# Performance work log

Hardware: AMD Instinct MI355X
Metric: run time of the kernel (lower is better)

The kernel has to match this reference:

```python
import jax, jax.numpy as jnp
import numpy as np

D_MODEL = 512
SEQ_LEN = 2048
S = 32  # local window size
BATCH = 2


def setup_inputs() -> dict:
    key = jax.random.key(0)
    ks = jax.random.split(key, 12)
    shp = (SEQ_LEN, BATCH, D_MODEL)
    return {
        "query": jax.random.normal(ks[0], shp, jnp.float32),
        "key": jax.random.normal(ks[1], shp, jnp.float32),
        "value": jax.random.normal(ks[2], shp, jnp.float32),
        "Wq": jax.random.normal(ks[3], (D_MODEL, D_MODEL), jnp.float32) * 0.02,
        "bq": jax.random.normal(ks[4], (D_MODEL,), jnp.float32) * 0.01,
        "Wk": jax.random.normal(ks[5], (D_MODEL, D_MODEL), jnp.float32) * 0.02,
        "bk": jax.random.normal(ks[6], (D_MODEL,), jnp.float32) * 0.01,
        "Wv": jax.random.normal(ks[7], (D_MODEL, D_MODEL), jnp.float32) * 0.02,
        "bv": jax.random.normal(ks[8], (D_MODEL,), jnp.float32) * 0.01,
        "pos_bias": jax.random.normal(ks[9], (SEQ_LEN, SEQ_LEN), jnp.float32) * 0.02,
        "Wo": jax.random.normal(ks[10], (D_MODEL, D_MODEL), jnp.float32) * 0.02,
        "bo": jax.random.normal(ks[11], (D_MODEL,), jnp.float32) * 0.01,
    }


def _aft_local(query, key, value, Wq, bq, Wk, bk, Wv, bv, pos_bias, Wo, bo):
    T, B, D = query.shape
    q = query @ Wq.T + bq  # [T,B,D]
    k = key @ Wk.T + bk
    v = value @ Wv.T + bv
    pb = pos_bias[:T, :T]

    # max_logit: elementwise max of per-dim key max and (key + col-max of pos_bias) max,
    # then batch index 0 (faithful to original `[0]` indexing) -> shape [D]
    max_logit = jnp.maximum(k.max(axis=0),
                            (k + pb.max(axis=0)[:, None, None]).max(axis=0))[0]

    # out-of-window running sums: tokens t' <= t - S contribute exp(k) (no pos bias)
    ek = jnp.exp(k - max_logit)                 # [T,B,D]
    cs_num = jnp.cumsum(ek * v, axis=0)
    cs_den = jnp.cumsum(ek, axis=0)
    t_arr = jnp.arange(T)
    prefix_idx = jnp.clip(t_arr - S, 0, T - 1)
    has_prefix = (t_arr >= S)[:, None, None]
    num_out = jnp.where(has_prefix, cs_num[prefix_idx], 0.0)
    den_out = jnp.where(has_prefix, cs_den[prefix_idx], 0.0)

    # in-window part: t' in [max(0, t-S+1), t] with pos_bias[t, t']
    j = jnp.arange(S)
    idx_raw = t_arr[:, None] - S + 1 + j[None, :]   # [T,S]
    valid = (idx_raw >= 0).astype(k.dtype)
    idx = jnp.clip(idx_raw, 0, T - 1)
    k_win = k[idx]                                  # [T,S,B,D]
    v_win = v[idx]                                  # [T,S,B,D]
    pb_win = pb[t_arr[:, None], idx]                # [T,S]
    exp_l = jnp.exp(k_win + pb_win[:, :, None, None] - max_logit) * valid[:, :, None, None]
    num_in = (exp_l * v_win).sum(axis=1)            # [T,B,D]
    den_in = exp_l.sum(axis=1)

    y = jax.nn.sigmoid(q) * (num_out + num_in) / (den_out + den_in)
    return y @ Wo.T + bo


def reference(query, key, value, Wq, bq, Wk, bk, Wv, bv, pos_bias, Wo, bo):
    return _aft_local(query, key, value, Wq, bq, Wk, bk, Wv, bv, pos_bias, Wo, bo)
```

## Files before the change

### kernel.cpp

```cpp
#include <hip/hip_runtime.h>
#include <hip/hip_bf16.h>

#define TT 2048
#define BB 2
#define DD 512
#define BD (BB*DD)
#define SS 32
#define MR (TT*BB)
#define NE (TT*BB*DD)
#define CH 32

typedef __bf16 bf16x8 __attribute__((ext_vector_type(8)));
typedef float f32x4 __attribute__((ext_vector_type(4)));

__device__ __forceinline__ void async_copy16(void* lds, const void* gptr) {
    __builtin_amdgcn_global_load_lds(
        (const __attribute__((address_space(1))) void*)gptr,
        (__attribute__((address_space(3))) void*)lds,
        16, 0, 0);
}

#define MFMA16(a,b,c) __builtin_amdgcn_mfma_f32_16x16x32_bf16((a),(b),(c),0,0,0)

__global__ __launch_bounds__(256) void cast_all(
    const float* __restrict__ s0, const float* __restrict__ s1, const float* __restrict__ s2,
    const float* __restrict__ w0, const float* __restrict__ w1,
    const float* __restrict__ w2, const float* __restrict__ w3,
    __hip_bfloat16* __restrict__ d0, __hip_bfloat16* __restrict__ d1, __hip_bfloat16* __restrict__ d2,
    __hip_bfloat16* __restrict__ e0, __hip_bfloat16* __restrict__ e1,
    __hip_bfloat16* __restrict__ e2, __hip_bfloat16* __restrict__ e3)
{
    int b = blockIdx.x;
    const float* s;
    __hip_bfloat16* d;
    size_t i;
    if (b < 6144) {
        int which = b >> 11;
        s = which == 0 ? s0 : (which == 1 ? s1 : s2);
        d = which == 0 ? d0 : (which == 1 ? d1 : d2);
        i = ((size_t)(b & 2047) * 256 + threadIdx.x) * 4;
    } else {
        int b2 = b - 6144;
        int which = b2 >> 8;
        s = which == 0 ? w0 : (which == 1 ? w1 : (which == 2 ? w2 : w3));
        d = which == 0 ? e0 : (which == 1 ? e1 : (which == 2 ? e2 : e3));
        i = ((size_t)(b2 & 255) * 256 + threadIdx.x) * 4;
    }
    float4 f = *(const float4*)(s + i);
    union { __hip_bfloat16 h[4]; ushort4 u; } cv;
    cv.h[0] = __float2bfloat16(f.x); cv.h[1] = __float2bfloat16(f.y);
    cv.h[2] = __float2bfloat16(f.z); cv.h[3] = __float2bfloat16(f.w);
    *(ushort4*)((unsigned short*)d + i) = cv.u;
}

__global__ __launch_bounds__(256) void gemm_qkv(
    const __hip_bfloat16* __restrict__ qb, const __hip_bfloat16* __restrict__ kb,
    const __hip_bfloat16* __restrict__ vb,
    const __hip_bfloat16* __restrict__ Wqb, const __hip_bfloat16* __restrict__ Wkb,
    const __hip_bfloat16* __restrict__ Wvb,
    const float* __restrict__ bq, const float* __restrict__ bk,
    const float* __restrict__ bv,
    float* __restrict__ qout, float* __restrict__ ekn,
    float* __restrict__ part)
{
    __shared__ char smem[49152];
    const int tid = threadIdx.x;
    const int lane = tid & 63;
    const int wv = tid >> 6;
    const int wave_m = wv >> 1, wave_n = wv & 1;
    const int m0 = blockIdx.y * 64, n0 = blockIdx.x * 64;
    const int kq = lane >> 4, rr = lane & 15;

    if (blockIdx.z == 0) {
        f32x4 acc[2][2] = {};
        const __hip_bfloat16* Arow = qb + (size_t)(m0 + lane) * DD + wv * 8;
        const __hip_bfloat16* Wrow = Wqb + (size_t)(n0 + lane) * DD + wv * 8;
        async_copy16(smem + 0*8192 +        wv*1024, Arow + 0);
        async_copy16(smem + 0*8192 + 4096 + wv*1024, Wrow + 0);
        async_copy16(smem + 1*8192 +        wv*1024, Arow + 32);
        async_copy16(smem + 1*8192 + 4096 + wv*1024, Wrow + 32);
        asm volatile("s_waitcnt vmcnt(2)" ::: "memory");
        __builtin_amdgcn_s_barrier();
        #pragma unroll
        for (int it = 0; it < 16; ++it) {
            if (it + 2 < 16) {
                char* nb = smem + ((it + 2) % 3) * 8192;
                async_copy16(nb +        wv*1024, Arow + (it+2)*32);
                async_copy16(nb + 4096 + wv*1024, Wrow + (it+2)*32);
            }
            const char* cb = smem + (it % 3) * 8192;
            bf16x8 a0 = *(const bf16x8*)(cb + kq*1024 + (wave_m*32 +  0 + rr)*16);
            bf16x8 a1 = *(const bf16x8*)(cb + kq*1024 + (wave_m*32 + 16 + rr)*16);
            bf16x8 w0 = *(const bf16x8*)(cb + 4096 + kq*1024 + (wave_n*32 +  0 + rr)*16);
            bf16x8 w1 = *(const bf16x8*)(cb + 4096 + kq*1024 + (wave_n*32 + 16 + rr)*16);
            acc[0][0] = MFMA16(a0, w0, acc[0][0]);
            acc[0][1] = MFMA16(a0, w1, acc[0][1]);
            acc[1][0] = MFMA16(a1, w0, acc[1][0]);
            acc[1][1] = MFMA16(a1, w1, acc[1][1]);
            if (it < 15) {
                if (it < 14) asm volatile("s_waitcnt vmcnt(2) lgkmcnt(0)" ::: "memory");
                else         asm volatile("s_waitcnt vmcnt(0) lgkmcnt(0)" ::: "memory");
                __builtin_amdgcn_s_barrier();
            }
        }
        #pragma unroll
        for (int ms = 0; ms < 2; ++ms)
            #pragma unroll
            for (int ns = 0; ns < 2; ++ns) {
                int n = n0 + wave_n*32 + ns*16 + rr;
                float bn = bq[n];
                #pragma unroll
                for (int r = 0; r < 4; ++r) {
                    int m = m0 + wave_m*32 + ms*16 + kq*4 + r;
                    qout[(size_t)m * DD + n] = acc[ms][ns][r] + bn;
                }
            }
    } else {
        f32x4 acck[2][2] = {}, accv[2][2] = {};
        const __hip_bfloat16* AKrow = kb + (size_t)(m0 + lane) * DD + wv * 8;
        const __hip_bfloat16* WKrow = Wkb + (size_t)(n0 + lane) * DD + wv * 8;
        const __hip_bfloat16* AVrow = vb + (size_t)(m0 + lane) * DD + wv * 8;
        const __hip_bfloat16* WVrow = Wvb + (size_t)(n0 + lane) * DD + wv * 8;
        #pragma unroll
        for (int pt = 0; pt < 2; ++pt) {
            char* nb = smem + pt * 16384;
            async_copy16(nb +         wv*1024, AKrow + pt*32);
            async_copy16(nb +  4096 + wv*1024, WKrow + pt*32);
            async_copy16(nb +  8192 + wv*1024, AVrow + pt*32);
            async_copy16(nb + 12288 + wv*1024, WVrow + pt*32);
        }
        asm volatile("s_waitcnt vmcnt(4)" ::: "memory");
        __builtin_amdgcn_s_barrier();
        #pragma unroll
        for (int it = 0; it < 16; ++it) {
            if (it + 2 < 16) {
                char* nb = smem + ((it + 2) % 3) * 16384;
                async_copy16(nb +         wv*1024, AKrow + (it+2)*32);
                async_copy16(nb +  4096 + wv*1024, WKrow + (it+2)*32);
                async_copy16(nb +  8192 + wv*1024, AVrow + (it+2)*32);
                async_copy16(nb + 12288 + wv*1024, WVrow + (it+2)*32);
            }
            const char* cb = smem + (it % 3) * 16384;
            bf16x8 ak0 = *(const bf16x8*)(cb +         kq*1024 + (wave_m*32 +  0 + rr)*16);
            bf16x8 ak1 = *(const bf16x8*)(cb +         kq*1024 + (wave_m*32 + 16 + rr)*16);
            bf16x8 bk0 = *(const bf16x8*)(cb +  4096 + kq*1024 + (wave_n*32 +  0 + rr)*16);
            bf16x8 bk1 = *(const bf16x8*)(cb +  4096 + kq*1024 + (wave_n*32 + 16 + rr)*16);
            bf16x8 av0 = *(const bf16x8*)(cb +  8192 + kq*1024 + (wave_m*32 +  0 + rr)*16);
            bf16x8 av1 = *(const bf16x8*)(cb +  8192 + kq*1024 + (wave_m*32 + 16 + rr)*16);
            bf16x8 bv0 = *(const bf16x8*)(cb + 12288 + kq*1024 + (wave_n*32 +  0 + rr)*16);
            bf16x8 bv1 = *(const bf16x8*)(cb + 12288 + kq*1024 + (wave_n*32 + 16 + rr)*16);
            acck[0][0] = MFMA16(ak0, bk0, acck[0][0]);
            acck[0][1] = MFMA16(ak0, bk1, acck[0][1]);
            acck[1][0] = MFMA16(ak1, bk0, acck[1][0]);
            acck[1][1] = MFMA16(ak1, bk1, acck[1][1]);
            accv[0][0] = MFMA16(av0, bv0, accv[0][0]);
            accv[0][1] = MFMA16(av0, bv1, accv[0][1]);
            accv[1][0] = MFMA16(av1, bv0, accv[1][0]);
            accv[1][1] = MFMA16(av1, bv1, accv[1][1]);
            if (it < 15) {
                if (it < 14) asm volatile("s_waitcnt vmcnt(4) lgkmcnt(0)" ::: "memory");
                else         asm volatile("s_waitcnt vmcnt(0) lgkmcnt(0)" ::: "memory");
                __builtin_amdgcn_s_barrier();
            }
        }
        float sd[2][2] = {{0.f,0.f},{0.f,0.f}};
        float sn[2][2] = {{0.f,0.f},{0.f,0.f}};
        #pragma unroll
        for (int ms = 0; ms < 2; ++ms)
            #pragma unroll
            for (int ns = 0; ns < 2; ++ns) {
                int n = n0 + wave_n*32 + ns*16 + rr;
                float bkn = bk[n], bvn = bv[n];
                #pragma unroll
                for (int r = 0; r < 4; ++r) {
                    int m = m0 + wave_m*32 + ms*16 + kq*4 + r;
                    float e  = expf(acck[ms][ns][r] + bkn);
                    float nv = e * (accv[ms][ns][r] + bvn);
                    float2 st; st.x = e; st.y = nv;
                    *(float2*)&ekn[((size_t)m * DD + n) * 2] = st;
                    sd[ns][r & 1] += e;
                    sn[ns][r & 1] += nv;
                }
            }
        #pragma unroll
        for (int ns = 0; ns < 2; ++ns)
            #pragma unroll
            for (int par = 0; par < 2; ++par) {
                sd[ns][par] += __shfl_xor(sd[ns][par], 16, 64);
                sd[ns][par] += __shfl_xor(sd[ns][par], 32, 64);
                sn[ns][par] += __shfl_xor(sn[ns][par], 16, 64);
                sn[ns][par] += __shfl_xor(sn[ns][par], 32, 64);
            }
        __syncthreads();
        float* red = (float*)smem;
        if (lane < 16) {
            #pragma unroll
            for (int ns = 0; ns < 2; ++ns) {
                int c = wave_n*32 + ns*16 + rr;
                red[(0*2 + wave_m)*64 + c] = sd[ns][0];
                red[(1*2 + wave_m)*64 + c] = sd[ns][1];
                red[(2*2 + wave_m)*64 + c] = sn[ns][0];
                red[(3*2 + wave_m)*64 + c] = sn[ns][1];
            }
        }
        __syncthreads();
        {
            int which = tid >> 6;
            int c = tid & 63;
            float s = red[(which*2 + 0)*64 + c] + red[(which*2 + 1)*64 + c];
            int b = which & 1;
            int sel = which >> 1;
            part[((size_t)blockIdx.y * BD + b*512 + n0 + c) * 2 + sel] = s;
        }
    }
}

__global__ __launch_bounds__(256) void fused_window(
    const float* __restrict__ q, const float* __restrict__ ekn,
    const float* __restrict__ part, const float* __restrict__ pb,
    __hip_bfloat16* __restrict__ yb)
{
    __shared__ float wl[CH][SS];
    const int tid = threadIdx.x;
    const int col = blockIdx.x * 256 + tid;
    const int chunk = blockIdx.y;
    const int t0 = chunk * CH;

    #pragma unroll
    for (int i = 0; i < (CH * SS) / 256; ++i) {
        int idx = tid + i * 256;
        int tl = idx >> 5, j = idx & 31;
        int t = t0 + tl;
        int u = t - (SS - 1) + j;
        float w = 0.f;
        if (u >= 0) w = expf(pb[(size_t)t * TT + u]);
        wl[tl][j] = w;
    }
    __syncthreads();

    float ring_d[32], ring_n[32];
    float cs_d = 0.f, cs_n = 0.f;
    const bool hasp = (chunk > 0);
    if (hasp) {
        float pd[4] = {0.f,0.f,0.f,0.f}, pn[4] = {0.f,0.f,0.f,0.f};
        int p = 0;
        for (; p + 4 <= chunk; p += 4) {
            #pragma unroll
            for (int u2 = 0; u2 < 4; ++u2) {
                float2 v = *(const float2*)&part[((size_t)(p + u2) * BD + col) * 2];
                pd[u2] += v.x; pn[u2] += v.y;
            }
        }
        for (; p < chunk; ++p) {
            float2 v = *(const float2*)&part[((size_t)p * BD + col) * 2];
            pd[0] += v.x; pn[0] += v.y;
        }
        float pref_d = (pd[0] + pd[1]) + (pd[2] + pd[3]);
        float pref_n = (pn[0] + pn[1]) + (pn[2] + pn[3]);
        float ssd = 0.f, ssn = 0.f;
        #pragma unroll
        for (int i = 0; i < 32; ++i) {
            float2 v = *(const float2*)&ekn[((size_t)(t0 - 32 + i) * BD + col) * 2];
            ring_d[i] = v.x; ring_n[i] = v.y;
            ssd += v.x; ssn += v.y;
        }
        cs_d = pref_d - ssd;
        cs_n = pref_n - ssn;
    } else {
        #pragma unroll
        for (int i = 0; i < 32; ++i) { ring_d[i] = 0.f; ring_n[i] = 0.f; }
    }

    #pragma unroll
    for (int s = 0; s < CH; ++s) {
        int t = t0 + s;
        size_t off = (size_t)t * BD + col;
        float2 env = *(const float2*)&ekn[off * 2];
        cs_d += ring_d[s];
        cs_n += ring_n[s];
        ring_d[s] = env.x;
        ring_n[s] = env.y;
        float den = 0.f, num = 0.f;
        #pragma unroll
        for (int j4 = 0; j4 < 8; ++j4) {
            float4 w4 = *(const float4*)&wl[s][j4 * 4];
            den += w4.x * ring_d[(s + 1 + j4*4 + 0) & 31];
            num += w4.x * ring_n[(s + 1 + j4*4 + 0) & 31];
            den += w4.y * ring_d[(s + 1 + j4*4 + 1) & 31];
            num += w4.y * ring_n[(s + 1 + j4*4 + 1) & 31];
            den += w4.z * ring_d[(s + 1 + j4*4 + 2) & 31];
            num += w4.z * ring_n[(s + 1 + j4*4 + 2) & 31];
            den += w4.w * ring_d[(s + 1 + j4*4 + 3) & 31];
            num += w4.w * ring_n[(s + 1 + j4*4 + 3) & 31];
        }
        if (hasp) { den += cs_d; num += cs_n; }
        float qv = q[off];
        float sig = 1.f / (1.f + expf(-qv));
        yb[off] = __float2bfloat16(sig * num / den);
    }
}

__global__ __launch_bounds__(256) void gemm_out(
    const __hip_bfloat16* __restrict__ yb, const __hip_bfloat16* __restrict__ Wob,
    const float* __restrict__ bo, float* __restrict__ out)
{
    __shared__ char smem[24576];
    const int tid = threadIdx.x;
    const int lane = tid & 63;
    const int wv = tid >> 6;
    const int wave_m = wv >> 1, wave_n = wv & 1;
    const int m0 = blockIdx.y * 64, n0 = blockIdx.x * 64;
    const int kq = lane >> 4, rr = lane & 15;

    f32x4 acc[2][2] = {};
    const __hip_bfloat16* Arow = yb + (size_t)(m0 + lane) * DD + wv * 8;
    const __hip_bfloat16* Wrow = Wob + (size_t)(n0 + lane) * DD + wv * 8;

    async_copy16(smem + 0*8192 +        wv*1024, Arow + 0);
    async_copy16(smem + 0*8192 + 4096 + wv*1024, Wrow + 0);
    async_copy16(smem + 1*8192 +        wv*1024, Arow + 32);
    async_copy16(smem + 1*8192 + 4096 + wv*1024, Wrow + 32);
    asm volatile("s_waitcnt vmcnt(2)" ::: "memory");
    __builtin_amdgcn_s_barrier();
    #pragma unroll
    for (int it = 0; it < 16; ++it) {
        if (it + 2 < 16) {
            char* nb = smem + ((it + 2) % 3) * 8192;
            async_copy16(nb +        wv*1024, Arow + (it+2)*32);
            async_copy16(nb + 4096 + wv*1024, Wrow + (it+2)*32);
        }
        const char* cb = smem + (it % 3) * 8192;
        bf16x8 a0 = *(const bf16x8*)(cb + kq*1024 + (wave_m*32 +  0 + rr)*16);
        bf16x8 a1 = *(const bf16x8*)(cb + kq*1024 + (wave_m*32 + 16 + rr)*16);
        bf16x8 w0 = *(const bf16x8*)(cb + 4096 + kq*1024 + (wave_n*32 +  0 + rr)*16);
        bf16x8 w1 = *(const bf16x8*)(cb + 4096 + kq*1024 + (wave_n*32 + 16 + rr)*16);
        acc[0][0] = MFMA16(a0, w0, acc[0][0]);
        acc[0][1] = MFMA16(a0, w1, acc[0][1]);
        acc[1][0] = MFMA16(a1, w0, acc[1][0]);
        acc[1][1] = MFMA16(a1, w1, acc[1][1]);
        if (it < 15) {
            if (it < 14) asm volatile("s_waitcnt vmcnt(2) lgkmcnt(0)" ::: "memory");
            else         asm volatile("s_waitcnt vmcnt(0) lgkmcnt(0)" ::: "memory");
            __builtin_amdgcn_s_barrier();
        }
    }
    #pragma unroll
    for (int ms = 0; ms < 2; ++ms)
        #pragma unroll
        for (int ns = 0; ns < 2; ++ns) {
            int n = n0 + wave_n*32 + ns*16 + rr;
            float bn = bo[n];
            #pragma unroll
            for (int r = 0; r < 4; ++r) {
                int m = m0 + wave_m*32 + ms*16 + kq*4 + r;
                out[(size_t)m * DD + n] = acc[ms][ns][r] + bn;
            }
        }
}

extern "C" void kernel_launch(void* const* d_in, const int* in_sizes, int n_in,
                              void* d_out, int out_size, void* d_ws, size_t ws_size,
                              hipStream_t stream) {
    const float* query = (const float*)d_in[0];
    const float* key   = (const float*)d_in[1];
    const float* value = (const float*)d_in[2];
    const float* Wq    = (const float*)d_in[3];
    const float* bq    = (const float*)d_in[4];
    const float* Wk    = (const float*)d_in[5];
    const float* bk    = (const float*)d_in[6];
    const float* Wv    = (const float*)d_in[7];
    const float* bv    = (const float*)d_in[8];
    const float* pb    = (const float*)d_in[9];
    const float* Wo    = (const float*)d_in[10];
    const float* bo    = (const float*)d_in[11];
    float* out = (float*)d_out;

    float* ws = (float*)d_ws;
    float* q    = ws;
    float* ekn  = ws + (size_t)NE;
    float* part = ws + (size_t)3 * NE;
    __hip_bfloat16* bfb = (__hip_bfloat16*)(part + 131072);
    __hip_bfloat16* qb  = bfb;
    __hip_bfloat16* kb  = bfb + (size_t)NE;
    __hip_bfloat16* vb  = bfb + (size_t)2 * NE;
    __hip_bfloat16* yb  = bfb + (size_t)3 * NE;
    __hip_bfloat16* Wqb = bfb + (size_t)4 * NE;
    __hip_bfloat16* Wkb = Wqb + 262144;
    __hip_bfloat16* Wvb = Wkb + 262144;
    __hip_bfloat16* Wob = Wvb + 262144;

    cast_all<<<7168, 256, 0, stream>>>(query, key, value, Wq, Wk, Wv, Wo,
                                       qb, kb, vb, Wqb, Wkb, Wvb, Wob);

    gemm_qkv<<<dim3(DD / 64, MR / 64, 2), 256, 0, stream>>>(
        qb, kb, vb, Wqb, Wkb, Wvb, bq, bk, bv,
        q, ekn, part);

    fused_window<<<dim3(BD / 256, TT / CH), 256, 0, stream>>>(
        q, ekn, part, pb, yb);

    gemm_out<<<dim3(DD / 64, MR / 64), 256, 0, stream>>>(yb, Wob, bo, out);
}
```

Baseline: 172.0 us.

## Precompute chunk prefix sums in a separate scan kernel and preload window registers

Adds a small scan_part kernel that turns the per-chunk partial sums into exclusive prefix sums. fused_window then reads one prefix value instead of summing up to 63 partials per column, which removes the quadratic reduction across chunks. The fused kernel also loads all 64 ekn values and 32 q values into registers up front and uses vector float2 arithmetic. The costs are an extra kernel launch, a tiny 4-block kernel that runs serially, and higher register pressure (launch_bounds 256,1).

```diff
diff --git a/kernel.cpp b/kernel.cpp
--- a/kernel.cpp
+++ b/kernel.cpp
@@ -12,6 +12,7 @@
 
 typedef __bf16 bf16x8 __attribute__((ext_vector_type(8)));
 typedef float f32x4 __attribute__((ext_vector_type(4)));
+typedef float f32x2 __attribute__((ext_vector_type(2)));
 
 __device__ __forceinline__ void async_copy16(void* lds, const void* gptr) {
     __builtin_amdgcn_global_load_lds(
@@ -215,9 +216,28 @@
     }
 }
 
-__global__ __launch_bounds__(256) void fused_window(
+__global__ __launch_bounds__(256, 1) void scan_part(
+    const float* __restrict__ part, float* __restrict__ pref)
+{
+    const int col = blockIdx.x * 256 + threadIdx.x;
+    f32x2 run = {0.f, 0.f};
+    #pragma unroll
+    for (int p0 = 0; p0 < 64; p0 += 8) {
+        f32x2 v[8];
+        #pragma unroll
+        for (int u = 0; u < 8; ++u)
+            v[u] = *(const f32x2*)&part[((size_t)(p0 + u) * BD + col) * 2];
+        #pragma unroll
+        for (int u = 0; u < 8; ++u) {
+            *(f32x2*)&pref[((size_t)(p0 + u) * BD + col) * 2] = run;
+            run += v[u];
+        }
+    }
+}
+
+__global__ __launch_bounds__(256, 1) void fused_window(
     const float* __restrict__ q, const float* __restrict__ ekn,
-    const float* __restrict__ part, const float* __restrict__ pb,
+    const float* __restrict__ pref, const float* __restrict__ pb,
     __hip_bfloat16* __restrict__ yb)
 {
     __shared__ float wl[CH][SS];
@@ -225,6 +245,24 @@
     const int col = blockIdx.x * 256 + tid;
     const int chunk = blockIdx.y;
     const int t0 = chunk * CH;
+
+    f32x2 E[64];
+    if (chunk > 0) {
+        #pragma unroll
+        for (int i = 0; i < 64; ++i)
+            E[i] = *(const f32x2*)&ekn[((size_t)(t0 - 32 + i) * BD + col) * 2];
+    } else {
+        #pragma unroll
+        for (int i = 0; i < 32; ++i) E[i] = (f32x2){0.f, 0.f};
+        #pragma unroll
+        for (int i = 32; i < 64; ++i)
+            E[i] = *(const f32x2*)&ekn[((size_t)(t0 - 32 + i) * BD + col) * 2];
+    }
+    f32x2 P = *(const f32x2*)&pref[((size_t)chunk * BD + col) * 2];
+    float qv[CH];
+    #pragma unroll
+    for (int s = 0; s < CH; ++s)
+        qv[s] = q[(size_t)(t0 + s) * BD + col];
 
     #pragma unroll
     for (int i = 0; i < (CH * SS) / 256; ++i) {
@@ -238,65 +276,24 @@
     }
     __syncthreads();
 
-    float ring_d[32], ring_n[32];
-    float cs_d = 0.f, cs_n = 0.f;
-    const bool hasp = (chunk > 0);
-    if (hasp) {
-        float pd[4] = {0.f,0.f,0.f,0.f}, pn[4] = {0.f,0.f,0.f,0.f};
-        int p = 0;
-        for (; p + 4 <= chunk; p += 4) {
-            #pragma unroll
-            for (int u2 = 0; u2 < 4; ++u2) {
-                float2 v = *(const float2*)&part[((size_t)(p + u2) * BD + col) * 2];
-                pd[u2] += v.x; pn[u2] += v.y;
-            }
-        }
-        for (; p < chunk; ++p) {
-            float2 v = *(const float2*)&part[((size_t)p * BD + col) * 2];
-            pd[0] += v.x; pn[0] += v.y;
-        }
-        float pref_d = (pd[0] + pd[1]) + (pd[2] + pd[3]);
-        float pref_n = (pn[0] + pn[1]) + (pn[2] + pn[3]);
-        float ssd = 0.f, ssn = 0.f;
-        #pragma unroll
-        for (int i = 0; i < 32; ++i) {
-            float2 v = *(const float2*)&ekn[((size_t)(t0 - 32 + i) * BD + col) * 2];
-            ring_d[i] = v.x; ring_n[i] = v.y;
-            ssd += v.x; ssn += v.y;
-        }
-        cs_d = pref_d - ssd;
-        cs_n = pref_n - ssn;
-    } else {
-        #pragma unroll
-        for (int i = 0; i < 32; ++i) { ring_d[i] = 0.f; ring_n[i] = 0.f; }
-    }
+    f32x2 cs = P;
+    #pragma unroll
+    for (int i = 0; i < 32; ++i) cs -= E[i];
 
     #pragma unroll
     for (int s = 0; s < CH; ++s) {
-        int t = t0 + s;
-        size_t off = (size_t)t * BD + col;
-        float2 env = *(const float2*)&ekn[off * 2];
-        cs_d += ring_d[s];
-        cs_n += ring_n[s];
-        ring_d[s] = env.x;
-        ring_n[s] = env.y;
-        float den = 0.f, num = 0.f;
+        cs += E[s];
+        f32x2 acc = cs;
         #pragma unroll
         for (int j4 = 0; j4 < 8; ++j4) {
             float4 w4 = *(const float4*)&wl[s][j4 * 4];
-            den += w4.x * ring_d[(s + 1 + j4*4 + 0) & 31];
-            num += w4.x * ring_n[(s + 1 + j4*4 + 0) & 31];
-            den += w4.y * ring_d[(s + 1 + j4*4 + 1) & 31];
-            num += w4.y * ring_n[(s + 1 + j4*4 + 1) & 31];
-            den += w4.z * ring_d[(s + 1 + j4*4 + 2) & 31];
-            num += w4.z * ring_n[(s + 1 + j4*4 + 2) & 31];
-            den += w4.w * ring_d[(s + 1 + j4*4 + 3) & 31];
-            num += w4.w * ring_n[(s + 1 + j4*4 + 3) & 31];
-        }
-        if (hasp) { den += cs_d; num += cs_n; }
-        float qv = q[off];
-        float sig = 1.f / (1.f + expf(-qv));
-        yb[off] = __float2bfloat16(sig * num / den);
+            acc += w4.x * E[s + 1 + j4*4 + 0];
+            acc += w4.y * E[s + 1 + j4*4 + 1];
+            acc += w4.z * E[s + 1 + j4*4 + 2];
+            acc += w4.w * E[s + 1 + j4*4 + 3];
+        }
+        float sig = 1.f / (1.f + expf(-qv[s]));
+        yb[(size_t)(t0 + s) * BD + col] = __float2bfloat16(sig * acc.y / acc.x);
     }
 }
 
@@ -379,7 +376,8 @@
     float* q    = ws;
     float* ekn  = ws + (size_t)NE;
     float* part = ws + (size_t)3 * NE;
-    __hip_bfloat16* bfb = (__hip_bfloat16*)(part + 131072);
+    float* pref = part + 131072;
+    __hip_bfloat16* bfb = (__hip_bfloat16*)(pref + 131072);
     __hip_bfloat16* qb  = bfb;
     __hip_bfloat16* kb  = bfb + (size_t)NE;
     __hip_bfloat16* vb  = bfb + (size_t)2 * NE;
@@ -396,8 +394,10 @@
         qb, kb, vb, Wqb, Wkb, Wvb, bq, bk, bv,
         q, ekn, part);
 
+    scan_part<<<4, 256, 0, stream>>>(part, pref);
+
     fused_window<<<dim3(BD / 256, TT / CH), 256, 0, stream>>>(
-        q, ekn, part, pb, yb);
+        q, ekn, pref, pb, yb);
 
     gemm_out<<<dim3(DD / 64, MR / 64), 256, 0, stream>>>(yb, Wob, bo, out);
 }
```

New measurement: 172.3 us. Within noise of the previous version (+0.1%).
